# Optimization experiments

Hardware: AMD Instinct MI355X
Metric: run time of the kernel (lower is better)

Reference implementation:

```python
import jax, jax.numpy as jnp
import numpy as np

NEG_SLOPE = 0.2


def gatv2(x, src, dst, Wl, Wr, att, b, concat):
    """PyG GATv2Conv (share_weights=False, default negative_slope=0.2).
    x: [N, Fin]; src/dst: [E] (self-loops already included);
    Wl/Wr: [Fin, H*D]; att: [H, D]; b: [H*D] if concat else [D].
    """
    N = x.shape[0]
    H, D = att.shape
    xl = (x @ Wl).reshape(N, H, D)  # source transform (messages)
    xr = (x @ Wr).reshape(N, H, D)  # target transform
    g = xl[src] + xr[dst]                                   # [E, H, D]
    e = jnp.einsum('ehd,hd->eh', jax.nn.leaky_relu(g, NEG_SLOPE), att)  # [E, H]
    # segment softmax over incoming edges of each dst node
    m = jax.ops.segment_max(e, dst, num_segments=N)         # [N, H]
    ex = jnp.exp(e - m[dst])
    s = jax.ops.segment_sum(ex, dst, num_segments=N)
    alpha = ex / (s[dst] + 1e-16)                           # [E, H]
    out = jax.ops.segment_sum(alpha[:, :, None] * xl[src], dst, num_segments=N)  # [N, H, D]
    out = out.reshape(N, H * D) if concat else out.mean(axis=1)
    return out + b


def _glorot(key, fan_in, shape):
    return jax.random.normal(key, shape, dtype=jnp.float32) / np.sqrt(fan_in)


def setup_inputs() -> dict:
    key = jax.random.key(0)
    N, E = 50000, 800000
    dim_in, dim_h, dim_out, heads = 128, 32, 16, 8
    hid = dim_h * heads  # 256
    ks = jax.random.split(key, 16)
    x = jax.random.normal(ks[0], (N, dim_in), dtype=jnp.float32)
    edge_index = jax.random.randint(ks[1], (2, E), 0, N, dtype=jnp.int32)
    p = {
        'Wl1': _glorot(ks[2], dim_in, (dim_in, hid)),
        'Wr1': _glorot(ks[3], dim_in, (dim_in, hid)),
        'att1': _glorot(ks[4], dim_h, (heads, dim_h)),
        'b1': jnp.zeros((hid,), jnp.float32),
        'Wl2': _glorot(ks[5], hid, (hid, hid)),
        'Wr2': _glorot(ks[6], hid, (hid, hid)),
        'att2': _glorot(ks[7], dim_h, (heads, dim_h)),
        'b2': jnp.zeros((hid,), jnp.float32),
        'Wl3': _glorot(ks[8], hid, (hid, hid)),
        'Wr3': _glorot(ks[9], hid, (hid, hid)),
        'att3': _glorot(ks[10], dim_h, (heads, dim_h)),
        'b3': jnp.zeros((hid,), jnp.float32),
        'Wl4': _glorot(ks[11], hid, (hid, dim_out)),
        'Wr4': _glorot(ks[12], hid, (hid, dim_out)),
        'att4': _glorot(ks[13], dim_out, (1, dim_out)),
        'b4': jnp.zeros((dim_out,), jnp.float32),
    }
    return {'x': x, 'edge_index': edge_index, **p}


def reference(x, edge_index,
              Wl1, Wr1, att1, b1,
              Wl2, Wr2, att2, b2,
              Wl3, Wr3, att3, b3,
              Wl4, Wr4, att4, b4):
    N = x.shape[0]
    # PyG GATv2Conv default add_self_loops=True
    loop = jnp.arange(N, dtype=edge_index.dtype)
    src = jnp.concatenate([edge_index[0], loop])
    dst = jnp.concatenate([edge_index[1], loop])
    # eval mode: dropout is identity (note: first dropout output is unused in source)
    h = gatv2(x, src, dst, Wl1, Wr1, att1, b1, concat=True)
    h = jax.nn.elu(h)
    h = gatv2(h, src, dst, Wl2, Wr2, att2, b2, concat=True)
    h = jax.nn.elu(h)
    h = gatv2(h, src, dst, Wl3, Wr3, att3, b3, concat=True)
    h = jax.nn.elu(h)
    h = gatv2(h, src, dst, Wl4, Wr4, att4, b4, concat=True)  # heads=1 -> same as concat
    return jax.nn.log_softmax(h, axis=1)
```

## Files before the change

### kernel.cpp

```cpp
#include <hip/hip_runtime.h>
#include <math.h>

#define NEG_SLOPE 0.2f

typedef _Float16 f16;
typedef _Float16 f16x2 __attribute__((ext_vector_type(2)));
typedef _Float16 f16x4 __attribute__((ext_vector_type(4)));
typedef _Float16 f16x8 __attribute__((ext_vector_type(8)));
typedef float f32x4 __attribute__((ext_vector_type(4)));

static inline int idiv(int a, int b) { return (a + b - 1) / b; }



__global__ __launch_bounds__(256) void conv_x_packed(const float* __restrict__ x,
                                                     f16* __restrict__ pa, int N) {
    int R = blockIdx.x;
    #pragma unroll
    for (int u = 0; u < 8; ++u) {
        int c = threadIdx.x + u * 256;
        int g = c >> 7, r = c & 127;
        int row = R * 128 + r;
        f16x8 v;
        if (row < N) {
            float4 a = *(const float4*)(x + (size_t)row * 128 + g * 8);
            float4 b = *(const float4*)(x + (size_t)row * 128 + g * 8 + 4);
            v = (f16x8){(f16)a.x, (f16)a.y, (f16)a.z, (f16)a.w,
                        (f16)b.x, (f16)b.y, (f16)b.z, (f16)b.w};
        } else {
            v = (f16x8){0, 0, 0, 0, 0, 0, 0, 0};
        }
        *(f16x8*)(pa + ((size_t)(R * 16 + g) * 128 + r) * 8) = v;
    }
}

__global__ __launch_bounds__(256) void convT_all(
    const float* __restrict__ W1l, const float* __restrict__ W1r,
    const float* __restrict__ W2l, const float* __restrict__ W2r,
    const float* __restrict__ W3l, const float* __restrict__ W3r,
    f16* __restrict__ P1l, f16* __restrict__ P1r,
    f16* __restrict__ P2l, f16* __restrict__ P2r,
    f16* __restrict__ P3l, f16* __restrict__ P3r) {
    __shared__ float tbl[32][33];
    const float* W;
    f16* P;
    int K;
    switch (blockIdx.z) {
        case 0: W = W1l; P = P1l; K = 128; break;
        case 1: W = W1r; P = P1r; K = 128; break;
        case 2: W = W2l; P = P2l; K = 256; break;
        case 3: W = W2r; P = P2r; K = 256; break;
        case 4: W = W3l; P = P3l; K = 256; break;
        default: W = W3r; P = P3r; K = 256; break;
    }
    int bk = blockIdx.x * 32, bc = blockIdx.y * 32;
    if (bk >= K) return;
    int tx = threadIdx.x & 31, ty = threadIdx.x >> 5;
    #pragma unroll
    for (int i = 0; i < 32; i += 8)
        tbl[ty + i][tx] = W[(size_t)(bk + ty + i) * 256 + bc + tx];
    __syncthreads();
    if (threadIdx.x < 128) {
        int cl = threadIdx.x & 31;
        int gl = threadIdx.x >> 5;
        int col = bc + cl;
        int g = (bk >> 3) + gl;
        f16x8 v;
        #pragma unroll
        for (int j = 0; j < 8; ++j) v[j] = (f16)tbl[gl * 8 + j][cl];
        *(f16x8*)(P + ((size_t)((col >> 7) * (K >> 3) + g) * 128 + (col & 127)) * 8) = v;
    }
}


__global__ void hist_kernel(const int* __restrict__ dst, int E, int N, int* __restrict__ cnt) {
    int i = blockIdx.x * blockDim.x + threadIdx.x;
    if (i >= E + N) return;
    int d = (i < E) ? dst[i] : (i - E);
    atomicAdd(&cnt[d], 1);
}

__global__ __launch_bounds__(256) void scanA(const int* __restrict__ cnt,
                                             int* __restrict__ bsum, int N) {
    __shared__ int ws[4];
    int tid = threadIdx.x, lane = tid & 63, wid = tid >> 6;
    int i0 = blockIdx.x * 1024 + tid * 4;
    int s = 0;
    if (i0 + 3 < N) {
        int4 v = *(const int4*)(cnt + i0);
        s = v.x + v.y + v.z + v.w;
    } else {
        for (int j = 0; j < 4; ++j)
            if (i0 + j < N) s += cnt[i0 + j];
    }
    #pragma unroll
    for (int o = 1; o < 64; o <<= 1) s += __shfl_xor(s, o);
    if (lane == 0) ws[wid] = s;
    __syncthreads();
    if (tid == 0) bsum[blockIdx.x] = ws[0] + ws[1] + ws[2] + ws[3];
}

__global__ __launch_bounds__(256) void scanB(int* __restrict__ bsum, int nb) {
    __shared__ int ws[4];
    int tid = threadIdx.x, lane = tid & 63, wid = tid >> 6;
    int v = (tid < nb) ? bsum[tid] : 0;
    int incl = v;
    #pragma unroll
    for (int o = 1; o < 64; o <<= 1) {
        int t = __shfl_up(incl, o);
        if (lane >= o) incl += t;
    }
    if (lane == 63) ws[wid] = incl;
    __syncthreads();
    int add = 0;
    for (int w = 0; w < wid; ++w) add += ws[w];
    if (tid < nb) bsum[tid] = add + incl - v;
}

__global__ __launch_bounds__(256) void scanC(const int* __restrict__ cnt,
                                             const int* __restrict__ bsum,
                                             int* __restrict__ rp, int* __restrict__ wofs, int N) {
    __shared__ int ws[4];
    __shared__ int base_s;
    int tid = threadIdx.x, lane = tid & 63, wid = tid >> 6;
    int i0 = blockIdx.x * 1024 + tid * 4;
    int v0 = (i0 + 0 < N) ? cnt[i0 + 0] : 0;
    int v1 = (i0 + 1 < N) ? cnt[i0 + 1] : 0;
    int v2 = (i0 + 2 < N) ? cnt[i0 + 2] : 0;
    int v3 = (i0 + 3 < N) ? cnt[i0 + 3] : 0;
    int t4 = v0 + v1 + v2 + v3;
    int incl = t4;
    #pragma unroll
    for (int o = 1; o < 64; o <<= 1) {
        int t = __shfl_up(incl, o);
        if (lane >= o) incl += t;
    }
    if (lane == 63) ws[wid] = incl;
    if (tid == 0) base_s = bsum[blockIdx.x];
    __syncthreads();
    int wadd = 0;
    for (int w = 0; w < wid; ++w) wadd += ws[w];
    int pre = base_s + wadd + incl - t4;
    int p1 = pre + v0, p2 = p1 + v1, p3 = p2 + v2, p4 = p3 + v3;
    if (i0 + 0 < N) { wofs[i0 + 0] = pre; rp[i0 + 1] = p1; }
    if (i0 + 1 < N) { wofs[i0 + 1] = p1;  rp[i0 + 2] = p2; }
    if (i0 + 2 < N) { wofs[i0 + 2] = p2;  rp[i0 + 3] = p3; }
    if (i0 + 3 < N) { wofs[i0 + 3] = p3;  rp[i0 + 4] = p4; }
    if (blockIdx.x == 0 && tid == 0) rp[0] = 0;
}

__global__ void scatter_kernel(const int* __restrict__ src, const int* __restrict__ dst,
                               int E, int N, int* __restrict__ wofs, int* __restrict__ sorted_src) {
    int i = blockIdx.x * blockDim.x + threadIdx.x;
    if (i >= E + N) return;
    int d, s;
    if (i < E) { d = dst[i]; s = src[i]; } else { d = i - E; s = d; }
    int pos = atomicAdd(&wofs[d], 1);
    sorted_src[pos] = s;
}


__device__ __forceinline__ void gll16(const f16* g, f16* l) {
#if __has_builtin(__builtin_amdgcn_global_load_lds)
    __builtin_amdgcn_global_load_lds((const __attribute__((address_space(1))) void*)g,
                                     (__attribute__((address_space(3))) void*)l, 16, 0, 0);
#else
    *(f16x8*)l = *(const f16x8*)g;
#endif
}

__global__ __launch_bounds__(256) void gemm16_packed(
    const f16* __restrict__ PA, int N, int K,
    const f16* __restrict__ PBl, const f16* __restrict__ PBr,
    f16* __restrict__ Cl, f16* __restrict__ Cr) {
    __shared__ f16 lds[2][2][8192];
    const int nblk = gridDim.x;
    int bid = blockIdx.x;
    int xcd = bid & 7, jj = bid >> 3;
    int nper = nblk >> 3, rem = nblk & 7;
    int slot = (xcd < rem) ? xcd * (nper + 1) + jj
                           : rem * (nper + 1) + (xcd - rem) * nper + jj;
    int R = slot >> 2, by = slot & 3;
    const f16* __restrict__ PB = (by >> 1) ? PBr : PBl;
    f16* __restrict__ C = (by >> 1) ? Cr : Cl;
    const int cb = by & 1;
    const int row0 = R * 128;
    const int col0 = cb * 128;
    const f16* Abase = PA + (size_t)R * 128 * K;
    const f16* Bbase = PB + (size_t)cb * 128 * K;
    const int t = threadIdx.x;
    const int lane = t & 63, wid = t >> 6;
    const int wr = (wid >> 1) * 64, wc = (wid & 1) * 64;
    const int lg = lane >> 4, lr = lane & 15;

    f32x4 acc[4][4];
    #pragma unroll
    for (int m = 0; m < 4; ++m)
        #pragma unroll
        for (int n = 0; n < 4; ++n) acc[m][n] = (f32x4){0.f, 0.f, 0.f, 0.f};

    auto stage = [&](int buf, int k0) {
        const f16* As = Abase + (size_t)k0 * 128 + t * 8;
        const f16* Bs = Bbase + (size_t)k0 * 128 + t * 8;
        f16* Al = &lds[buf][0][t * 8];
        f16* Bl = &lds[buf][1][t * 8];
        #pragma unroll
        for (int u = 0; u < 4; ++u) gll16(As + u * 2048, Al + u * 2048);
        #pragma unroll
        for (int u = 0; u < 4; ++u) gll16(Bs + u * 2048, Bl + u * 2048);
    };

    const int nk = K >> 6;
    stage(0, 0);
    asm volatile("s_waitcnt vmcnt(0)" ::: "memory");
    __syncthreads();
    for (int c = 0; c < nk; ++c) {
        if (c + 1 < nk) stage((c + 1) & 1, (c + 1) * 64);
        f16x8* Asp = (f16x8*)lds[c & 1][0];
        f16x8* Bsp = (f16x8*)lds[c & 1][1];
        #pragma unroll
        for (int s = 0; s < 2; ++s) {
            f16x8 af[4], bf[4];
            #pragma unroll
            for (int m = 0; m < 4; ++m) af[m] = Asp[(s * 4 + lg) * 128 + wr + m * 16 + lr];
            #pragma unroll
            for (int n = 0; n < 4; ++n) bf[n] = Bsp[(s * 4 + lg) * 128 + wc + n * 16 + lr];
            #pragma unroll
            for (int m = 0; m < 4; ++m)
                #pragma unroll
                for (int n = 0; n < 4; ++n)
                    acc[m][n] = __builtin_amdgcn_mfma_f32_16x16x32_f16(af[m], bf[n], acc[m][n], 0, 0, 0);
        }
        asm volatile("s_waitcnt vmcnt(0)" ::: "memory");
        __syncthreads();
    }
    #pragma unroll
    for (int m = 0; m < 4; ++m) {
        int row_b = row0 + wr + m * 16 + lg * 4;
        #pragma unroll
        for (int reg = 0; reg < 4; ++reg) {
            int row = row_b + reg;
            if (row < N) {
                #pragma unroll
                for (int n = 0; n < 4; ++n)
                    C[(size_t)row * 256 + col0 + wc + n * 16 + lr] = (f16)acc[m][n][reg];
            }
        }
    }
}


__global__ __launch_bounds__(256) void gemm_small16(
    const f16* __restrict__ A, int N,
    const float* __restrict__ Wl, const float* __restrict__ Wr,
    float* __restrict__ Cl, float* __restrict__ Cr) {
    const int K = 256, M = 16;
    __shared__ float As[16][260];
    __shared__ float Ws[256 * 16];
    const float* __restrict__ W = (blockIdx.y == 0) ? Wl : Wr;
    float* __restrict__ C = (blockIdx.y == 0) ? Cl : Cr;
    int row0 = blockIdx.x * 16;
    int tid = threadIdx.x;
    {
        #pragma unroll
        for (int u = 0; u < 4; ++u)
            *(float4*)&Ws[tid * 16 + u * 4] = *(const float4*)(W + tid * 16 + u * 4);
        int r = tid >> 4;
        int c = (tid & 15) * 16;
        int row = row0 + r;
        if (row < N) {
            int R = row >> 7, rr = row & 127;
            const f16* base = A + ((size_t)(R * 32 + (c >> 3)) * 128 + rr) * 8;
            f16x8 v0 = *(const f16x8*)base;
            f16x8 v1 = *(const f16x8*)(base + 1024);
            #pragma unroll
            for (int j = 0; j < 8; ++j) {
                As[r][c + j] = (float)v0[j];
                As[r][c + 8 + j] = (float)v1[j];
            }
        } else {
            #pragma unroll
            for (int j = 0; j < 16; ++j) As[r][c + j] = 0.f;
        }
    }
    __syncthreads();
    int r = tid >> 4;
    int col = tid & 15;
    float acc = 0.f;
    #pragma unroll 8
    for (int k = 0; k < K; ++k) acc = fmaf(As[r][k], Ws[k * M + col], acc);
    int row = row0 + r;
    if (row < N) C[(size_t)row * M + col] = acc;
}


__global__ __launch_bounds__(256) void edge_h8_f16(
    const f16* __restrict__ xl, const f16* __restrict__ xr,
    const int* __restrict__ rp, const int* __restrict__ ss,
    const float* __restrict__ att, const float* __restrict__ bias,
    f16* __restrict__ hout, int N) {
    int tid = threadIdx.x;
    int half = tid >> 5;
    int hl = tid & 31;
    int n = blockIdx.x * 8 + half;
    if (n >= N) return;
    const int HD = 256;
    f16x8 xrr = *(const f16x8*)(xr + (size_t)n * HD + hl * 8);
    float4 atlo = *(const float4*)(att + hl * 8);
    float4 athi = *(const float4*)(att + hl * 8 + 4);
    f16x2 at01 = {(f16)atlo.x, (f16)atlo.y};
    f16x2 at23 = {(f16)atlo.z, (f16)atlo.w};
    f16x2 at45 = {(f16)athi.x, (f16)athi.y};
    f16x2 at67 = {(f16)athi.z, (f16)athi.w};
    const f16 ns = (f16)NEG_SLOPE;
    float m = -INFINITY, s = 0.f;
    float a[8];
    #pragma unroll
    for (int j = 0; j < 8; ++j) a[j] = 0.f;
    int beg = rp[n], end = rp[n + 1];
    int last = end - 1;
    const f16* xb = xl + hl * 8;
    f16x8 r0 = *(const f16x8*)(xb + (size_t)ss[beg] * HD);
    f16x8 r1 = *(const f16x8*)(xb + (size_t)ss[min(beg + 1, last)] * HD);
    f16x8 r2 = *(const f16x8*)(xb + (size_t)ss[min(beg + 2, last)] * HD);
    f16x8 r3 = *(const f16x8*)(xb + (size_t)ss[min(beg + 3, last)] * HD);
    int j4 = ss[min(beg + 4, last)];
    int j5 = ss[min(beg + 5, last)];

    auto score = [&](const f16x8& cur) -> float {
        f16x8 g = cur + xrr;
        f16x8 gs = g * ns;
        f16x8 lk = __builtin_elementwise_max(g, gs);
#if __has_builtin(__builtin_amdgcn_fdot2)
        f16x2 l01 = __builtin_shufflevector(lk, lk, 0, 1);
        f16x2 l23 = __builtin_shufflevector(lk, lk, 2, 3);
        f16x2 l45 = __builtin_shufflevector(lk, lk, 4, 5);
        f16x2 l67 = __builtin_shufflevector(lk, lk, 6, 7);
        float p = __builtin_amdgcn_fdot2(l01, at01, 0.f, false);
        p = __builtin_amdgcn_fdot2(l23, at23, p, false);
        p = __builtin_amdgcn_fdot2(l45, at45, p, false);
        p = __builtin_amdgcn_fdot2(l67, at67, p, false);
#else
        float p = (float)lk[0] * atlo.x + (float)lk[1] * atlo.y +
                  (float)lk[2] * atlo.z + (float)lk[3] * atlo.w +
                  (float)lk[4] * athi.x + (float)lk[5] * athi.y +
                  (float)lk[6] * athi.z + (float)lk[7] * athi.w;
#endif
        return p;
    };

    int i = beg;
    for (; i + 1 < end; i += 2) {
        f16x8 c0 = r0, c1 = r1;
        r0 = r2; r1 = r3;
        r2 = *(const f16x8*)(xb + (size_t)j4 * HD);
        r3 = *(const f16x8*)(xb + (size_t)j5 * HD);
        j4 = ss[min(i + 6, last)];
        j5 = ss[min(i + 7, last)];
        float p0 = score(c0);
        float p1 = score(c1);
        p0 += __shfl_xor(p0, 1);
        p1 += __shfl_xor(p1, 1);
        p0 += __shfl_xor(p0, 2);
        p1 += __shfl_xor(p1, 2);
        float d0 = p0 - m, d1 = p1 - m;
        if (__any(fmaxf(d0, d1) > 8.f)) {
            float mn = fmaxf(m, fmaxf(p0, p1));
            float cf = __expf(m - mn);
            s *= cf;
            #pragma unroll
            for (int j = 0; j < 8; ++j) a[j] *= cf;
            m = mn;
            d0 = p0 - m; d1 = p1 - m;
        }
        float e0 = __expf(d0);
        float e1 = __expf(d1);
        s += e0 + e1;
        #pragma unroll
        for (int j = 0; j < 8; ++j)
            a[j] = fmaf(e1, (float)c1[j], fmaf(e0, (float)c0[j], a[j]));
    }
    if (i < end) {
        f16x8 c0 = r0;
        float p0 = score(c0);
        p0 += __shfl_xor(p0, 1);
        p0 += __shfl_xor(p0, 2);
        float d0 = p0 - m;
        if (__any(d0 > 8.f)) {
            float mn = fmaxf(m, p0);
            float cf = __expf(m - mn);
            s *= cf;
            #pragma unroll
            for (int j = 0; j < 8; ++j) a[j] *= cf;
            m = mn;
            d0 = p0 - m;
        }
        float e0 = __expf(d0);
        s += e0;
        #pragma unroll
        for (int j = 0; j < 8; ++j) a[j] = fmaf(e0, (float)c0[j], a[j]);
    }
    float inv = 1.f / (s + 1e-16f);
    float4 blo = *(const float4*)(bias + hl * 8);
    float4 bhi = *(const float4*)(bias + hl * 8 + 4);
    float o[8];
    o[0] = a[0] * inv + blo.x; o[1] = a[1] * inv + blo.y;
    o[2] = a[2] * inv + blo.z; o[3] = a[3] * inv + blo.w;
    o[4] = a[4] * inv + bhi.x; o[5] = a[5] * inv + bhi.y;
    o[6] = a[6] * inv + bhi.z; o[7] = a[7] * inv + bhi.w;
    f16x8 ov;
    #pragma unroll
    for (int j = 0; j < 8; ++j) {
        float e = o[j] > 0.f ? o[j] : __expf(o[j]) - 1.f;
        ov[j] = (f16)e;
    }
    *(f16x8*)(hout + ((size_t)((n >> 7) * 32 + hl) * 128 + (n & 127)) * 8) = ov;
}


__global__ __launch_bounds__(256) void edge_h1_kernel(
    const float* __restrict__ xl, const float* __restrict__ xr,
    const int* __restrict__ rp, const int* __restrict__ ss,
    const float* __restrict__ att, const float* __restrict__ bias,
    float* __restrict__ out, int N) {
    int tid = threadIdx.x;
    int grp = tid >> 4;
    int gl = tid & 15;
    int n = blockIdx.x * 16 + grp;
    if (n >= N) return;
    float xrv = xr[(size_t)n * 16 + gl];
    float attv = att[gl];
    float bv = bias[gl];
    float m = -INFINITY, s = 0.f, acc = 0.f;
    int beg = rp[n], end = rp[n + 1], last = end - 1;
    const float* xb = xl + gl;
    float x0 = xb[(size_t)ss[beg] * 16];
    float x1 = xb[(size_t)ss[min(beg + 1, last)] * 16];
    float x2 = xb[(size_t)ss[min(beg + 2, last)] * 16];
    float x3 = xb[(size_t)ss[min(beg + 3, last)] * 16];
    int j4 = ss[min(beg + 4, last)];
    int j5 = ss[min(beg + 5, last)];
    int i = beg;
    for (; i + 1 < end; i += 2) {
        float c0 = x0, c1 = x1;
        x0 = x2; x1 = x3;
        x2 = xb[(size_t)j4 * 16];
        x3 = xb[(size_t)j5 * 16];
        j4 = ss[min(i + 6, last)];
        j5 = ss[min(i + 7, last)];
        float g0 = c0 + xrv, g1 = c1 + xrv;
        float p0 = attv * fmaxf(g0, NEG_SLOPE * g0);
        float p1 = attv * fmaxf(g1, NEG_SLOPE * g1);
        p0 += __shfl_xor(p0, 1); p1 += __shfl_xor(p1, 1);
        p0 += __shfl_xor(p0, 2); p1 += __shfl_xor(p1, 2);
        p0 += __shfl_xor(p0, 4); p1 += __shfl_xor(p1, 4);
        p0 += __shfl_xor(p0, 8); p1 += __shfl_xor(p1, 8);
        float d0 = p0 - m, d1 = p1 - m;
        if (__any(fmaxf(d0, d1) > 8.f)) {
            float mn = fmaxf(m, fmaxf(p0, p1));
            float cf = __expf(m - mn);
            s *= cf; acc *= cf;
            m = mn;
            d0 = p0 - m; d1 = p1 - m;
        }
        float e0 = __expf(d0), e1 = __expf(d1);
        s += e0 + e1;
        acc = fmaf(e1, c1, fmaf(e0, c0, acc));
    }
    if (i < end) {
        float c0 = x0;
        float g0 = c0 + xrv;
        float p0 = attv * fmaxf(g0, NEG_SLOPE * g0);
        p0 += __shfl_xor(p0, 1);
        p0 += __shfl_xor(p0, 2);
        p0 += __shfl_xor(p0, 4);
        p0 += __shfl_xor(p0, 8);
        float d0 = p0 - m;
        if (__any(d0 > 8.f)) {
            float mn = fmaxf(m, p0);
            float cf = __expf(m - mn);
            s *= cf; acc *= cf;
            m = mn;
            d0 = p0 - m;
        }
        float e0 = __expf(d0);
        s += e0;
        acc = fmaf(e0, c0, acc);
    }
    float v = acc / (s + 1e-16f) + bv;
    float mx = v;
    mx = fmaxf(mx, __shfl_xor(mx, 1));
    mx = fmaxf(mx, __shfl_xor(mx, 2));
    mx = fmaxf(mx, __shfl_xor(mx, 4));
    mx = fmaxf(mx, __shfl_xor(mx, 8));
    float ex = __expf(v - mx);
    float se = ex;
    se += __shfl_xor(se, 1);
    se += __shfl_xor(se, 2);
    se += __shfl_xor(se, 4);
    se += __shfl_xor(se, 8);
    out[(size_t)n * 16 + gl] = v - mx - __logf(se);
}


extern "C" void kernel_launch(void* const* d_in, const int* in_sizes, int n_in,
                              void* d_out, int out_size, void* d_ws, size_t ws_size,
                              hipStream_t stream) {
    const float* x    = (const float*)d_in[0];
    const int*   ei   = (const int*)d_in[1];
    const float* Wl1  = (const float*)d_in[2];
    const float* Wr1  = (const float*)d_in[3];
    const float* att1 = (const float*)d_in[4];
    const float* b1   = (const float*)d_in[5];
    const float* Wl2  = (const float*)d_in[6];
    const float* Wr2  = (const float*)d_in[7];
    const float* att2 = (const float*)d_in[8];
    const float* b2   = (const float*)d_in[9];
    const float* Wl3  = (const float*)d_in[10];
    const float* Wr3  = (const float*)d_in[11];
    const float* att3 = (const float*)d_in[12];
    const float* b3   = (const float*)d_in[13];
    const float* Wl4  = (const float*)d_in[14];
    const float* Wr4  = (const float*)d_in[15];
    const float* att4 = (const float*)d_in[16];
    const float* b4   = (const float*)d_in[17];

    const int N = in_sizes[0] / 128;
    const int E = in_sizes[1] / 2;
    const int* src = ei;
    const int* dst = ei + E;
    const int Etot = E + N;
    const int ntile = idiv(N, 128);

    char* wsb = (char*)d_ws;
    size_t off = 0;
    auto alloc = [&](size_t bytes) -> void* {
        void* p = wsb + off;
        off += (bytes + 255) & ~(size_t)255;
        return p;
    };
    f16*   PX   = (f16*)alloc((size_t)ntile * 128 * 128 * 2);
    f16*   PH   = (f16*)alloc((size_t)ntile * 128 * 256 * 2);
    f16*   xl16 = (f16*)alloc((size_t)N * 256 * 2);
    f16*   xr16 = (f16*)alloc((size_t)N * 256 * 2);
    float* xl4  = (float*)alloc((size_t)N * 16 * 4);
    float* xr4  = (float*)alloc((size_t)N * 16 * 4);
    f16*   PB1l = (f16*)alloc((size_t)256 * 128 * 2);
    f16*   PB1r = (f16*)alloc((size_t)256 * 128 * 2);
    f16*   PB2l = (f16*)alloc((size_t)256 * 256 * 2);
    f16*   PB2r = (f16*)alloc((size_t)256 * 256 * 2);
    f16*   PB3l = (f16*)alloc((size_t)256 * 256 * 2);
    f16*   PB3r = (f16*)alloc((size_t)256 * 256 * 2);
    int*   cnt  = (int*)alloc((size_t)N * 4);
    int*   wof  = (int*)alloc((size_t)N * 4);
    int*   rp   = (int*)alloc((size_t)(N + 1) * 4);
    int*   ss   = (int*)alloc((size_t)Etot * 4);
    int*   bsum = (int*)alloc((size_t)idiv(N, 1024) * 4);

    conv_x_packed<<<ntile, 256, 0, stream>>>(x, PX, N);
    convT_all<<<dim3(8, 8, 6), 256, 0, stream>>>(Wl1, Wr1, Wl2, Wr2, Wl3, Wr3,
                                                 PB1l, PB1r, PB2l, PB2r, PB3l, PB3r);

    hipMemsetAsync(cnt, 0, (size_t)N * 4, stream);
    hist_kernel<<<idiv(Etot, 256), 256, 0, stream>>>(dst, E, N, cnt);
    const int nb = idiv(N, 1024);
    scanA<<<nb, 256, 0, stream>>>(cnt, bsum, N);
    scanB<<<1, 256, 0, stream>>>(bsum, nb);
    scanC<<<nb, 256, 0, stream>>>(cnt, bsum, rp, wof, N);
    scatter_kernel<<<idiv(Etot, 256), 256, 0, stream>>>(src, dst, E, N, wof, ss);

    const int nblk = ntile * 4;
    gemm16_packed<<<nblk, 256, 0, stream>>>(PX, N, 128, PB1l, PB1r, xl16, xr16);
    edge_h8_f16<<<idiv(N, 8), 256, 0, stream>>>(xl16, xr16, rp, ss, att1, b1, PH, N);
    gemm16_packed<<<nblk, 256, 0, stream>>>(PH, N, 256, PB2l, PB2r, xl16, xr16);
    edge_h8_f16<<<idiv(N, 8), 256, 0, stream>>>(xl16, xr16, rp, ss, att2, b2, PH, N);
    gemm16_packed<<<nblk, 256, 0, stream>>>(PH, N, 256, PB3l, PB3r, xl16, xr16);
    edge_h8_f16<<<idiv(N, 8), 256, 0, stream>>>(xl16, xr16, rp, ss, att3, b3, PH, N);
    gemm_small16<<<dim3(idiv(N, 16), 2), 256, 0, stream>>>(PH, N, Wl4, Wr4, xl4, xr4);
    edge_h1_kernel<<<idiv(N, 16), 256, 0, stream>>>(xl4, xr4, rp, ss, att4, b4, (float*)d_out, N);
}
```

Before: 444.2 us.

## Sort nodes by degree and split edge attention kernel per head

Adds a degree-bucketed node permutation (histogram, scan, scatter over degrees capped at 63) so that lanes in a wave process nodes of similar in-degree, reducing divergence in the per-node edge loops. The head-dim edge kernel is restructured so each block handles a single head for 64 nodes, with 4 lanes per node-head instead of 32 lanes per node. This gives each wave 16 independent nodes and shorter shuffle reductions. The cost is three extra small kernels, a permutation gather, and less contiguous gathers of source rows, since each head's 64-byte slice is fetched separately.

```diff
diff --git a/kernel.cpp b/kernel.cpp
--- a/kernel.cpp
+++ b/kernel.cpp
@@ -157,6 +157,35 @@
     if (i < E) { d = dst[i]; s = src[i]; } else { d = i - E; s = d; }
     int pos = atomicAdd(&wofs[d], 1);
     sorted_src[pos] = s;
+}
+
+
+__global__ void deg_hist(const int* __restrict__ rp, int N, int* __restrict__ dcnt) {
+    int i = blockIdx.x * blockDim.x + threadIdx.x;
+    if (i >= N) return;
+    int deg = rp[i + 1] - rp[i];
+    atomicAdd(&dcnt[min(deg, 63)], 1);
+}
+
+__global__ void deg_scan(int* __restrict__ dcnt) {
+    int tid = threadIdx.x;
+    int v = dcnt[tid];
+    int incl = v;
+    #pragma unroll
+    for (int o = 1; o < 64; o <<= 1) {
+        int t = __shfl_up(incl, o);
+        if (tid >= o) incl += t;
+    }
+    dcnt[tid] = incl - v;
+}
+
+__global__ void deg_scatter(const int* __restrict__ rp, int N, int* __restrict__ dofs,
+                            int* __restrict__ perm) {
+    int i = blockIdx.x * blockDim.x + threadIdx.x;
+    if (i >= N) return;
+    int deg = min(rp[i + 1] - rp[i], 63);
+    int pos = atomicAdd(&dofs[deg], 1);
+    perm[pos] = i;
 }
 
 
@@ -294,20 +323,26 @@
 }
 
 
-__global__ __launch_bounds__(256) void edge_h8_f16(
+__global__ __launch_bounds__(256) void edge_h8_split(
     const f16* __restrict__ xl, const f16* __restrict__ xr,
     const int* __restrict__ rp, const int* __restrict__ ss,
+    const int* __restrict__ perm,
     const float* __restrict__ att, const float* __restrict__ bias,
     f16* __restrict__ hout, int N) {
+    int bid = blockIdx.x;
+    int h = bid & 7;
+    int tile = bid >> 3;
     int tid = threadIdx.x;
-    int half = tid >> 5;
-    int hl = tid & 31;
-    int n = blockIdx.x * 8 + half;
-    if (n >= N) return;
+    int lane = tid & 63, wave = tid >> 6;
+    int task = tile * 64 + wave * 16 + (lane >> 2);
+    if (task >= N) return;
+    int n = perm[task];
+    int ll = lane & 3;
+    const int doff = h * 32 + ll * 8;
     const int HD = 256;
-    f16x8 xrr = *(const f16x8*)(xr + (size_t)n * HD + hl * 8);
-    float4 atlo = *(const float4*)(att + hl * 8);
-    float4 athi = *(const float4*)(att + hl * 8 + 4);
+    f16x8 xrr = *(const f16x8*)(xr + (size_t)n * HD + doff);
+    float4 atlo = *(const float4*)(att + doff);
+    float4 athi = *(const float4*)(att + doff + 4);
     f16x2 at01 = {(f16)atlo.x, (f16)atlo.y};
     f16x2 at23 = {(f16)atlo.z, (f16)atlo.w};
     f16x2 at45 = {(f16)athi.x, (f16)athi.y};
@@ -319,7 +354,7 @@
     for (int j = 0; j < 8; ++j) a[j] = 0.f;
     int beg = rp[n], end = rp[n + 1];
     int last = end - 1;
-    const f16* xb = xl + hl * 8;
+    const f16* xb = xl + doff;
     f16x8 r0 = *(const f16x8*)(xb + (size_t)ss[beg] * HD);
     f16x8 r1 = *(const f16x8*)(xb + (size_t)ss[min(beg + 1, last)] * HD);
     f16x8 r2 = *(const f16x8*)(xb + (size_t)ss[min(beg + 2, last)] * HD);
@@ -401,8 +436,8 @@
         for (int j = 0; j < 8; ++j) a[j] = fmaf(e0, (float)c0[j], a[j]);
     }
     float inv = 1.f / (s + 1e-16f);
-    float4 blo = *(const float4*)(bias + hl * 8);
-    float4 bhi = *(const float4*)(bias + hl * 8 + 4);
+    float4 blo = *(const float4*)(bias + doff);
+    float4 bhi = *(const float4*)(bias + doff + 4);
     float o[8];
     o[0] = a[0] * inv + blo.x; o[1] = a[1] * inv + blo.y;
     o[2] = a[2] * inv + blo.z; o[3] = a[3] * inv + blo.w;
@@ -414,20 +449,22 @@
         float e = o[j] > 0.f ? o[j] : __expf(o[j]) - 1.f;
         ov[j] = (f16)e;
     }
-    *(f16x8*)(hout + ((size_t)((n >> 7) * 32 + hl) * 128 + (n & 127)) * 8) = ov;
+    *(f16x8*)(hout + ((size_t)((n >> 7) * 32 + (4 * h + ll)) * 128 + (n & 127)) * 8) = ov;
 }
 
 
 __global__ __launch_bounds__(256) void edge_h1_kernel(
     const float* __restrict__ xl, const float* __restrict__ xr,
     const int* __restrict__ rp, const int* __restrict__ ss,
+    const int* __restrict__ perm,
     const float* __restrict__ att, const float* __restrict__ bias,
     float* __restrict__ out, int N) {
     int tid = threadIdx.x;
     int grp = tid >> 4;
     int gl = tid & 15;
-    int n = blockIdx.x * 16 + grp;
-    if (n >= N) return;
+    int task = blockIdx.x * 16 + grp;
+    if (task >= N) return;
+    int n = perm[task];
     float xrv = xr[(size_t)n * 16 + gl];
     float attv = att[gl];
     float bv = bias[gl];
@@ -556,26 +593,33 @@
     int*   rp   = (int*)alloc((size_t)(N + 1) * 4);
     int*   ss   = (int*)alloc((size_t)Etot * 4);
     int*   bsum = (int*)alloc((size_t)idiv(N, 1024) * 4);
+    int*   dcnt = (int*)alloc(64 * 4);
+    int*   perm = (int*)alloc((size_t)N * 4);
 
     conv_x_packed<<<ntile, 256, 0, stream>>>(x, PX, N);
     convT_all<<<dim3(8, 8, 6), 256, 0, stream>>>(Wl1, Wr1, Wl2, Wr2, Wl3, Wr3,
                                                  PB1l, PB1r, PB2l, PB2r, PB3l, PB3r);
 
     hipMemsetAsync(cnt, 0, (size_t)N * 4, stream);
+    hipMemsetAsync(dcnt, 0, 64 * 4, stream);
     hist_kernel<<<idiv(Etot, 256), 256, 0, stream>>>(dst, E, N, cnt);
     const int nb = idiv(N, 1024);
     scanA<<<nb, 256, 0, stream>>>(cnt, bsum, N);
     scanB<<<1, 256, 0, stream>>>(bsum, nb);
     scanC<<<nb, 256, 0, stream>>>(cnt, bsum, rp, wof, N);
     scatter_kernel<<<idiv(Etot, 256), 256, 0, stream>>>(src, dst, E, N, wof, ss);
+    deg_hist<<<idiv(N, 256), 256, 0, stream>>>(rp, N, dcnt);
+    deg_scan<<<1, 64, 0, stream>>>(dcnt);
+    deg_scatter<<<idiv(N, 256), 256, 0, stream>>>(rp, N, dcnt, perm);
 
     const int nblk = ntile * 4;
+    const int egrid = idiv(N, 64) * 8;
     gemm16_packed<<<nblk, 256, 0, stream>>>(PX, N, 128, PB1l, PB1r, xl16, xr16);
-    edge_h8_f16<<<idiv(N, 8), 256, 0, stream>>>(xl16, xr16, rp, ss, att1, b1, PH, N);
+    edge_h8_split<<<egrid, 256, 0, stream>>>(xl16, xr16, rp, ss, perm, att1, b1, PH, N);
     gemm16_packed<<<nblk, 256, 0, stream>>>(PH, N, 256, PB2l, PB2r, xl16, xr16);
-    edge_h8_f16<<<idiv(N, 8), 256, 0, stream>>>(xl16, xr16, rp, ss, att2, b2, PH, N);
+    edge_h8_split<<<egrid, 256, 0, stream>>>(xl16, xr16, rp, ss, perm, att2, b2, PH, N);
     gemm16_packed<<<nblk, 256, 0, stream>>>(PH, N, 256, PB3l, PB3r, xl16, xr16);
-    edge_h8_f16<<<idiv(N, 8), 256, 0, stream>>>(xl16, xr16, rp, ss, att3, b3, PH, N);
+    edge_h8_split<<<egrid, 256, 0, stream>>>(xl16, xr16, rp, ss, perm, att3, b3, PH, N);
     gemm_small16<<<dim3(idiv(N, 16), 2), 256, 0, stream>>>(PH, N, Wl4, Wr4, xl4, xr4);
-    edge_h1_kernel<<<idiv(N, 16), 256, 0, stream>>>(xl4, xr4, rp, ss, att4, b4, (float*)d_out, N);
-}
+    edge_h1_kernel<<<idiv(N, 16), 256, 0, stream>>>(xl4, xr4, rp, ss, perm, att4, b4, (float*)d_out, N);
+}
```

Result: slower. 914.0 us (+105.8%).
